# Performance work log

Measured on AMD Instinct MI355X. Metric: run time of the kernel, lower is better.

The kernel has to match this reference:

```python
import jax, jax.numpy as jnp
import numpy as np

MC = 16384
IND_T = 96
N_MAT = 4
N_STRIKES = 21


def _init_linear(key, fan_in, fan_out, prefix=()):
    k1, k2 = jax.random.split(key)
    lim = 1.0 / np.sqrt(fan_in)
    W = jax.random.uniform(k1, prefix + (fan_in, fan_out), minval=-lim, maxval=lim, dtype=jnp.float32)
    b = jax.random.uniform(k2, prefix + (fan_out,), minval=-lim, maxval=lim, dtype=jnp.float32)
    return W, b


def setup_inputs() -> dict:
    key = jax.random.key(0)
    ks = jax.random.split(key, 14)
    z = jax.random.normal(ks[0], (MC, IND_T), dtype=jnp.float32)
    zz = jax.random.normal(ks[1], (MC, IND_T), dtype=jnp.float32)
    timegrid = jnp.arange(IND_T + 1, dtype=jnp.float32) / 365.0  # daily grid
    maturities = jnp.array([24, 48, 72, 96], dtype=jnp.int32)    # in days
    strikes = jnp.linspace(0.8, 1.2, N_STRIKES, dtype=jnp.float32)
    sv_W1, sv_b1 = _init_linear(ks[2], 3, 100)
    sv_W2, sv_b2 = _init_linear(ks[3], 100, 100)
    sv_W3, sv_b3 = _init_linear(ks[4], 100, 1)
    vh_W1, vh_b1 = _init_linear(ks[5], 2, 20, (N_MAT,))
    vh_W2, vh_b2 = _init_linear(ks[6], 20, N_STRIKES, (N_MAT,))
    vd_W1, vd_b1 = _init_linear(ks[7], 1, 20)
    vd_W2, vd_b2 = _init_linear(ks[8], 20, 1)
    vv_W1, vv_b1 = _init_linear(ks[9], 1, 20)
    vv_W2, vv_b2 = _init_linear(ks[10], 20, 1)
    v0 = jax.random.uniform(ks[11], (1,), dtype=jnp.float32) * 0.1
    rho = jnp.ones((1,), dtype=jnp.float32) * -2.0
    return dict(S0=jnp.float32(1.0), rate=jnp.float32(0.05), z=z, zz=zz,
                timegrid=timegrid, strikes=strikes, v0=v0, rho=rho,
                sv_W1=sv_W1, sv_b1=sv_b1, sv_W2=sv_W2, sv_b2=sv_b2, sv_W3=sv_W3, sv_b3=sv_b3,
                vh_W1=vh_W1, vh_b1=vh_b1, vh_W2=vh_W2, vh_b2=vh_b2,
                vd_W1=vd_W1, vd_b1=vd_b1, vd_W2=vd_W2, vd_b2=vd_b2,
                vv_W1=vv_W1, vv_b1=vv_b1, vv_W2=vv_W2, vv_b2=vv_b2,
                maturities=maturities)


def reference(S0, rate, z, zz, timegrid, strikes, v0, rho,
              sv_W1, sv_b1, sv_W2, sv_b2, sv_W3, sv_b3,
              vh_W1, vh_b1, vh_W2, vh_b2,
              vd_W1, vd_b1, vd_W2, vd_b2,
              vv_W1, vv_b1, vv_W2, vv_b2,
              maturities):
    sg = jax.lax.stop_gradient
    mc = z.shape[0]
    n_mat = vh_W1.shape[0]
    n_strikes = strikes.shape[0]

    def s_vol(x):  # [MC,3] -> [MC,1], softplus output
        h1 = jax.nn.relu(x @ sv_W1 + sv_b1)
        h2 = jax.nn.relu(h1 @ sv_W2 + sv_b2)
        return jax.nn.softplus(h2 @ sv_W3 + sv_b3)

    def v_drift(v):  # [MC,1] -> [MC,1]
        return jax.nn.relu(v @ vd_W1 + vd_b1) @ vd_W2 + vd_b2

    def v_vol(v):  # [MC,1] -> [MC,1], softplus output
        return jax.nn.softplus(jax.nn.relu(v @ vv_W1 + vv_b1) @ vv_W2 + vv_b2)

    def vanilla_hedge_all(x):  # [MC,2] -> [MC, n_strikes, n_mat] (one net per maturity)
        h1 = jax.nn.relu(jnp.einsum('mi,kio->kmo', x, vh_W1) + vh_b1[:, None, :])
        out = jax.nn.softplus(jnp.einsum('kmo,koj->kmj', h1, vh_W2) + vh_b2[:, None, :])
        return jnp.transpose(out, (1, 2, 0))

    rho_t = jnp.tanh(rho)[0]
    days = jnp.round(timegrid * 365.0).astype(jnp.int32)       # [IND_T+1]
    le = days[1:, None] <= maturities[None, :]                  # [IND_T, n_mat]
    idx_net = jnp.argmax(le, axis=1)                            # first live maturity per step
    is_mat = jnp.any(days[1:, None] == maturities[None, :], axis=1)
    mat_idx = jnp.arange(n_mat)

    Slog0 = jnp.log(jnp.full((mc, 1), S0, dtype=jnp.float32))
    V0 = jnp.full((mc, 1), 1.0, dtype=jnp.float32) * jax.nn.sigmoid(v0)[0] * 0.5
    cv0 = jnp.zeros((mc, n_strikes, n_mat), dtype=jnp.float32)
    pv0 = jnp.zeros((n_mat, n_strikes), dtype=jnp.float32)

    xs = (z.T[:, :, None], zz.T[:, :, None], timegrid[:-1], timegrid[1:], idx_net, is_mat)

    def step(carry, x):
        Slog_old, V_old, cv, pv_h, pv_var = carry
        z_i, zz_i, t0, t1, idx, im = x
        h = t1 - t0
        sqh = jnp.sqrt(h)
        dW = sqh * z_i                                          # [MC,1]
        dB = rho_t * dW + jnp.sqrt(1.0 - rho_t ** 2) * sqh * zz_i
        ones_t = jnp.full((mc, 1), 1.0, dtype=jnp.float32) * t0
        pd = s_vol(jnp.concatenate([ones_t, Slog_old, V_old], axis=1))  # price diffusion
        cv_fwd = vanilla_hedge_all(jnp.concatenate([ones_t, sg(Slog_old)], axis=1))
        V_new = V_old + v_drift(V_old) * h + v_vol(V_old) * dB
        drift = rate - 0.5 * pd ** 2
        diff = pd * dW
        drift_c = 1.0 + jnp.abs(sg(drift)) * sqh                # tamed Euler
        diff_c = 1.0 + jnp.abs(sg(pd)) * sqh
        Slog_new = Slog_old + drift * h / drift_c + diff / diff_c
        S_new = jnp.exp(Slog_new)
        S_old = jnp.exp(Slog_old)
        dS = jnp.exp(-rate * t1) * S_new - jnp.exp(-rate * t0) * S_old  # [MC,1]
        mask = (mat_idx >= idx).astype(cv.dtype)                # live maturities only
        cv = cv + mask[None, None, :] * cv_fwd * sg(dS)[:, :, None]
        # hedged vanilla (call) prices collected at maturity steps
        payoff = jnp.exp(-rate * t1) * jnp.maximum(S_new - strikes[None, :], 0.0)
        price = payoff - cv[:, :, idx]                          # [MC, n_strikes]
        pv = jnp.mean(price, axis=0)
        pvar = jnp.var(price, axis=0, ddof=1)
        sel = (mat_idx == idx)[:, None] & im
        pv_h = jnp.where(sel, pv[None, :], pv_h)
        pv_var = jnp.where(sel, pvar[None, :], pv_var)
        return (Slog_new, V_new, cv, pv_h, pv_var), None

    (_, _, _, pv_h, pv_var), _ = jax.lax.scan(step, (Slog0, V0, cv0, pv0, pv0), xs)
    return jnp.stack([pv_h, pv_var])  # [2, n_mat, n_strikes]
```

## Files before the change

### kernel.cpp

```cpp
#include <hip/hip_runtime.h>
#include <hip/hip_bf16.h>
#include <math.h>


#define MC      16384
#define NSTEP   96
#define BLOCK   512
#define NGROUP  512
#define NPAIR   84

typedef short bf16x8 __attribute__((ext_vector_type(8)));
typedef float f32x4  __attribute__((ext_vector_type(4)));

union U8 { uint4 u; bf16x8 v; };
union BF2U { __hip_bfloat162 b; unsigned u; };

__device__ __forceinline__ unsigned bf16rne(float x) {
    unsigned u = __float_as_uint(x);
    return (u + 0x7FFFu + ((u >> 16) & 1u)) >> 16;
}
__device__ __forceinline__ unsigned pk2(float lo, float hi) {
    BF2U t; t.b = __float22bfloat162_rn(make_float2(lo, hi));
    return t.u;
}
__device__ __forceinline__ float sp(float x) {
    return fmaxf(x, 0.f) + __logf(1.f + __expf(-fabsf(x)));
}

__global__ __launch_bounds__(BLOCK, 4)
void lsv_sim(const float* __restrict__ S0p,   const float* __restrict__ ratep,
             const float* __restrict__ z,     const float* __restrict__ zzg,
             const float* __restrict__ strikesg,
             const float* __restrict__ v0p,   const float* __restrict__ rhop,
             const float* __restrict__ svW1,  const float* __restrict__ svb1,
             const float* __restrict__ svW2,  const float* __restrict__ svb2,
             const float* __restrict__ svW3,  const float* __restrict__ svb3,
             const float* __restrict__ vhW1,  const float* __restrict__ vhb1,
             const float* __restrict__ vhW2,  const float* __restrict__ vhb2,
             const float* __restrict__ vdW1,  const float* __restrict__ vdb1,
             const float* __restrict__ vdW2,  const float* __restrict__ vdb2,
             const float* __restrict__ vvW1,  const float* __restrict__ vvb1,
             const float* __restrict__ vvW2,  const float* __restrict__ vvb2,
             const int*   __restrict__ mats,
             float* __restrict__ psum, float* __restrict__ psq)
{
    __shared__ __align__(16) unsigned short H1c[16 * 32 * 8];
    __shared__ __align__(16) float W1f[16 * 32];
    __shared__ __align__(16) float WH1f[16 * 32];
    __shared__ __align__(16) float B2T[128], W3T[128];
    __shared__ __align__(16) float RED[32 * 4];
    __shared__ __align__(16) float VDl[2][32], VVl[2][32];
    __shared__ __align__(16) float PSs[2][32], PSq[2][32];
    __shared__ __align__(16) float VW[128];
    __shared__ __align__(16) float4 STEP[NSTEP];
    __shared__ float D1T[NSTEP];
    __shared__ int   ITAB[NSTEP];

    const int tid  = threadIdx.x;
    const int lane = tid & 63;
    const int w    = __builtin_amdgcn_readfirstlane(tid >> 6);
    const int quad = lane >> 4;
    const int col  = lane & 15;
    const int lp   = lane & 31;
    const int gpath = blockIdx.x * 32 + lp;

    const int pt = w & 1;
    const int jg = w >> 1;
    const int hm = w >> 1;

    for (int e = tid; e < 128; e += BLOCK) {
        float v = 0.f;
        if      (e < 20)             v = vdW1[e];
        else if (e < 40)             v = vdb1[e - 20];
        else if (e < 60)             v = vdW2[e - 40];
        else if (e >= 64 && e < 84)  v = vvW1[e - 64];
        else if (e >= 84 && e < 104) v = vvb1[e - 84];
        else if (e >= 104 && e < 124)v = vvW2[e - 104];
        else if (e == 124)           v = vdb2[0];
        else if (e == 125)           v = vvb2[0];
        VW[e] = v;
        B2T[e] = (e < 100) ? svb2[e] : 0.f;
        W3T[e] = (e < 100) ? svW3[e] : 0.f;
    }
    for (int e = tid; e < 512; e += BLOCK) {
        const int kc2 = e >> 5, r5 = e & 31, grp = r5 >> 3, kk = kc2 * 8 + (r5 & 7);
        float v = 0.f;
        if (kk < 100) v = (grp == 0) ? svW1[kk] : (grp == 1) ? svW1[100 + kk]
                        : (grp == 2) ? svW1[200 + kk] : svb1[kk];
        W1f[e] = v;
    }
    for (int e = tid; e < 512; e += BLOCK) {
        const int hq = e >> 5, r5 = e & 31, grp = r5 >> 3;
        const int hmm = hq >> 2, qq = hq & 3;
        const int j = qq * 8 + (r5 & 7);
        float v = 0.f;
        if (j < 20 && grp < 3)
            v = (grp == 0) ? vhW1[hmm * 40 + j] : (grp == 1) ? vhW1[hmm * 40 + 20 + j]
                                                : vhb1[hmm * 20 + j];
        WH1f[e] = v;
    }

    const float rate  = ratep[0];
    const float S0    = S0p[0];
    const float rho_t = tanhf(rhop[0]);
    const float srho  = sqrtf(1.f - rho_t * rho_t);
    const float b3    = svb3[0];

    if (tid < NSTEP) {
        const int i = tid;
        const float t0 = (float)i       * (1.f / 365.f);
        const float t1 = (float)(i + 1) * (1.f / 365.f);
        const float h  = t1 - t0;
        STEP[i] = make_float4(t0, h, sqrtf(h), __expf(-rate * t0));
        D1T[i]  = __expf(-rate * t1);
        const int day = i + 1;
        const int m0 = mats[0], m1 = mats[1], m2 = mats[2], m3 = mats[3];
        const int idx = (day > m0) + (day > m1) + (day > m2);
        const int mi  = (idx == 0) ? m0 : (idx == 1) ? m1 : (idx == 2) ? m2 : m3;
        ITAB[i] = idx | ((day == mi) ? 256 : 0);
    }

    bf16x8 Af[4][2];
#pragma unroll
    for (int c = 0; c < 4; c++)
#pragma unroll
        for (int t = 0; t < 2; t++) {
            U8 tt;
#pragma unroll
            for (int e2 = 0; e2 < 4; e2++) {
                const int k0 = 32 * c + 8 * quad + 2 * e2;
                const int j  = (2 * jg + t) * 16 + col;
                const float v0 = (k0     < 100 && j < 100) ? svW2[k0 * 100 + j]       : 0.f;
                const float v1 = (k0 + 1 < 100 && j < 100) ? svW2[(k0 + 1) * 100 + j] : 0.f;
                (&tt.u.x)[e2] = bf16rne(v0) | (bf16rne(v1) << 16);
            }
            Af[c][t] = tt.v;
        }
    bf16x8 Ah[2];
#pragma unroll
    for (int st = 0; st < 2; st++) {
        U8 tt;
#pragma unroll
        for (int e2 = 0; e2 < 4; e2++) {
            const int j0 = 8 * quad + 2 * e2, j1 = j0 + 1;
            const int s  = st * 16 + col;
            const float v0 = (j0 < 20 && s < 21) ? vhW2[hm * 420 + j0 * 21 + s] : 0.f;
            const float v1 = (j1 < 20 && s < 21) ? vhW2[hm * 420 + j1 * 21 + s] : 0.f;
            (&tt.u.x)[e2] = bf16rne(v0) | (bf16rne(v1) << 16);
        }
        Ah[st] = tt.v;
    }
    f32x4 c0h, c1h;
    float K0a[4], K1a[4];
#pragma unroll
    for (int r = 0; r < 4; r++) {
        const int s0 = quad * 4 + r, s1 = 16 + quad * 4 + r;
        c0h[r] = vhb2[hm * 21 + s0];
        K0a[r] = strikesg[s0];
        c1h[r] = (s1 < 21) ? vhb2[hm * 21 + s1] : 0.f;
        K1a[r] = (s1 < 21) ? strikesg[s1] : 1e30f;
    }

    float Slog = __logf(S0);
    float S    = __expf(Slog);
    float V    = (1.f / (1.f + __expf(-v0p[0]))) * 0.5f;
    f32x4 cv0 = {0.f, 0.f, 0.f, 0.f};
    f32x4 cv1 = {0.f, 0.f, 0.f, 0.f};
    float Slog_prev = 0.f, dS_prev = 0.f;

    const float* zrow  = z   + (size_t)gpath * NSTEP;
    const float* zzrow = zzg + (size_t)gpath * NSTEP;

    const int path = pt * 16 + col;
    const int kc   = jg * 4 + quad;

    __syncthreads();

    const int j0e = (2 * jg) * 16 + quad * 4;
    const float4 b2a = *reinterpret_cast<const float4*>(B2T + j0e);
    const float4 w3a = *reinterpret_cast<const float4*>(W3T + j0e);
    const float4 b2b = *reinterpret_cast<const float4*>(B2T + j0e + 16);
    const float4 w3b = *reinterpret_cast<const float4*>(W3T + j0e + 16);

    auto hedge_step = [&](int ip) {
        const int iv   = ITAB[ip];
        const int idxp = iv & 0xff;
        if (hm >= idxp) {
            const float t0p = STEP[ip].x;
            const float slp = __shfl(Slog_prev, path);
            U8 b;
#pragma unroll
            for (int hh = 0; hh < 2; hh++) {
                const float* Wp = WH1f + (hm * 4 + quad) * 32 + hh * 4;
                const float4 wt4 = *reinterpret_cast<const float4*>(Wp);
                const float4 ws4 = *reinterpret_cast<const float4*>(Wp + 8);
                const float4 bb4 = *reinterpret_cast<const float4*>(Wp + 16);
                const float x0 = fmaxf(bb4.x + t0p * wt4.x + slp * ws4.x, 0.f);
                const float x1 = fmaxf(bb4.y + t0p * wt4.y + slp * ws4.y, 0.f);
                const float x2 = fmaxf(bb4.z + t0p * wt4.z + slp * ws4.z, 0.f);
                const float x3 = fmaxf(bb4.w + t0p * wt4.w + slp * ws4.w, 0.f);
                (&b.u.x)[2 * hh]     = pk2(x0, x1);
                (&b.u.x)[2 * hh + 1] = pk2(x2, x3);
            }
            const f32x4 D0 = __builtin_amdgcn_mfma_f32_16x16x32_bf16(Ah[0], b.v, c0h, 0, 0, 0);
            const f32x4 D1 = __builtin_amdgcn_mfma_f32_16x16x32_bf16(Ah[1], b.v, c1h, 0, 0, 0);
            const float dsP = __shfl(dS_prev, path);
#pragma unroll
            for (int r = 0; r < 4; r++) {
                cv0[r] += sp(D0[r]) * dsP;
                cv1[r] += sp(D1[r]) * dsP;
            }
            if ((iv & 256) && hm == idxp) {
                const float Sp   = __shfl(S, path);
                const float d1p  = D1T[ip];
                float p0[4], q0[4], p1[4], q1[4];
#pragma unroll
                for (int r = 0; r < 4; r++) {
                    p0[r] = d1p * fmaxf(Sp - K0a[r], 0.f) - cv0[r];
                    p1[r] = d1p * fmaxf(Sp - K1a[r], 0.f) - cv1[r];
                    q0[r] = p0[r] * p0[r];
                    q1[r] = p1[r] * p1[r];
                }
#pragma unroll
                for (int o = 1; o <= 8; o <<= 1) {
#pragma unroll
                    for (int r = 0; r < 4; r++) {
                        p0[r] += __shfl_xor(p0[r], o);
                        q0[r] += __shfl_xor(q0[r], o);
                        p1[r] += __shfl_xor(p1[r], o);
                        q1[r] += __shfl_xor(q1[r], o);
                    }
                }
                if (col == 0) {
#pragma unroll
                    for (int r = 0; r < 4; r++) {
                        const int s0 = quad * 4 + r, s1 = 16 + quad * 4 + r;
                        PSs[pt][s0] = p0[r];  PSq[pt][s0] = q0[r];
                        if (s1 < 21) { PSs[pt][s1] = p1[r];  PSq[pt][s1] = q1[r]; }
                    }
                }
            }
        }
    };

    auto ps_reduce = [&](int ip) {
        if (w == 0) {
            const int iv = ITAB[ip];
            if (iv & 256) {
                const int s = lane & 31;
                if (s < 21) {
                    const float* src = (lane >= 32) ? &PSq[0][0] : &PSs[0][0];
                    const float acc = src[s] + src[32 + s];
                    float* dst = (lane >= 32) ? psq : psum;
                    dst[((iv & 0xff) * 21 + s) * NGROUP + blockIdx.x] = acc;
                }
            }
        }
    };

    for (int i = 0; i < NSTEP; i++) {
        const float zi  = zrow[i];
        const float zzi = zzrow[i];
        const float4 u  = STEP[i];

        {
            const float slp = __shfl(Slog, path);
            const float vp  = __shfl(V, path);
            const float t0  = u.x;
            const float* Wp = W1f + kc * 32;
            uint4 o;
#pragma unroll
            for (int hh = 0; hh < 2; hh++) {
                const float4 a4 = *reinterpret_cast<const float4*>(Wp + hh * 4);
                const float4 b4 = *reinterpret_cast<const float4*>(Wp + 8 + hh * 4);
                const float4 c4 = *reinterpret_cast<const float4*>(Wp + 16 + hh * 4);
                const float4 d4 = *reinterpret_cast<const float4*>(Wp + 24 + hh * 4);
                const float x0 = fmaxf(d4.x + t0 * a4.x + slp * b4.x + vp * c4.x, 0.f);
                const float x1 = fmaxf(d4.y + t0 * a4.y + slp * b4.y + vp * c4.y, 0.f);
                const float x2 = fmaxf(d4.z + t0 * a4.z + slp * b4.z + vp * c4.z, 0.f);
                const float x3 = fmaxf(d4.w + t0 * a4.w + slp * b4.w + vp * c4.w, 0.f);
                (&o.x)[2 * hh]     = pk2(x0, x1);
                (&o.x)[2 * hh + 1] = pk2(x2, x3);
            }
            *reinterpret_cast<uint4*>(H1c + (kc * 32 + path) * 8) = o;
        }
        if (i > 0) hedge_step(i - 1);
        if (w == 0) {
            float a2 = 0.f;
#pragma unroll
            for (int q5 = 0; q5 < 5; q5++) {
                const float4 w1 = *reinterpret_cast<const float4*>(VW + 4 * q5);
                const float4 b1 = *reinterpret_cast<const float4*>(VW + 20 + 4 * q5);
                const float4 w2 = *reinterpret_cast<const float4*>(VW + 40 + 4 * q5);
                a2 += fmaxf(V * w1.x + b1.x, 0.f) * w2.x;
                a2 += fmaxf(V * w1.y + b1.y, 0.f) * w2.y;
                a2 += fmaxf(V * w1.z + b1.z, 0.f) * w2.z;
                a2 += fmaxf(V * w1.w + b1.w, 0.f) * w2.w;
            }
            if (lane < 32) VDl[i & 1][lane] = a2;
        }
        if (w == 1) {
            float a2 = 0.f;
#pragma unroll
            for (int q5 = 0; q5 < 5; q5++) {
                const float4 w1 = *reinterpret_cast<const float4*>(VW + 64 + 4 * q5);
                const float4 b1 = *reinterpret_cast<const float4*>(VW + 84 + 4 * q5);
                const float4 w2 = *reinterpret_cast<const float4*>(VW + 104 + 4 * q5);
                a2 += fmaxf(V * w1.x + b1.x, 0.f) * w2.x;
                a2 += fmaxf(V * w1.y + b1.y, 0.f) * w2.y;
                a2 += fmaxf(V * w1.z + b1.z, 0.f) * w2.z;
                a2 += fmaxf(V * w1.w + b1.w, 0.f) * w2.w;
            }
            if (lane < 32) VVl[i & 1][lane] = a2;
        }
        __syncthreads();

        {
            f32x4 d0 = {0.f, 0.f, 0.f, 0.f};
            f32x4 d1 = {0.f, 0.f, 0.f, 0.f};
#pragma unroll
            for (int c = 0; c < 4; c++) {
                const bf16x8 b = *reinterpret_cast<const bf16x8*>(
                    H1c + ((quad + 4 * c) * 32 + path) * 8);
                d0 = __builtin_amdgcn_mfma_f32_16x16x32_bf16(Af[c][0], b, d0, 0, 0, 0);
                d1 = __builtin_amdgcn_mfma_f32_16x16x32_bf16(Af[c][1], b, d1, 0, 0, 0);
            }
            float acc = fmaxf(d0[0] + b2a.x, 0.f) * w3a.x
                      + fmaxf(d0[1] + b2a.y, 0.f) * w3a.y
                      + fmaxf(d0[2] + b2a.z, 0.f) * w3a.z
                      + fmaxf(d0[3] + b2a.w, 0.f) * w3a.w
                      + fmaxf(d1[0] + b2b.x, 0.f) * w3b.x
                      + fmaxf(d1[1] + b2b.y, 0.f) * w3b.y
                      + fmaxf(d1[2] + b2b.z, 0.f) * w3b.z
                      + fmaxf(d1[3] + b2b.w, 0.f) * w3b.w;
            acc += __shfl_xor(acc, 16);
            acc += __shfl_xor(acc, 32);
            if (quad == 0)
                RED[path * 4 + jg] = acc;
        }
        if (i > 0) ps_reduce(i - 1);
        __syncthreads();

        {
            const float4 rr = *reinterpret_cast<const float4*>(RED + lp * 4);
            const float pout = (rr.x + rr.y) + (rr.z + rr.w);
            const float pd = sp(pout + b3);
            const float vdv = VDl[i & 1][lp] + VW[124];
            const float vvv = sp(VVl[i & 1][lp] + VW[125]);
            const float sqh = u.z;
            const float dW = sqh * zi;
            const float dB = rho_t * dW + srho * sqh * zzi;
            const float Vn = V + vdv * u.y + vvv * dB;
            const float drift   = rate - 0.5f * pd * pd;
            const float diff    = pd * dW;
            const float drift_c = 1.f + fabsf(drift) * sqh;
            const float diff_c  = 1.f + fabsf(pd) * sqh;
            const float Sln = Slog + __fdividef(drift * u.y, drift_c) + __fdividef(diff, diff_c);
            const float Sn  = __expf(Sln);
            const float dS  = D1T[i] * Sn - u.w * S;
            Slog_prev = Slog; dS_prev = dS;
            Slog = Sln; S = Sn; V = Vn;
        }
    }

    hedge_step(NSTEP - 1);
    __syncthreads();
    ps_reduce(NSTEP - 1);
}

__global__ void lsv_finalize(const float* __restrict__ psum,
                             const float* __restrict__ psq,
                             float* __restrict__ out)
{
    const int t    = blockIdx.x;
    const int lane = threadIdx.x;
    float s = 0.f, q = 0.f;
    for (int b = lane; b < NGROUP; b += 64) {
        s += psum[t * NGROUP + b];
        q += psq [t * NGROUP + b];
    }
#pragma unroll
    for (int o = 1; o <= 32; o <<= 1) {
        s += __shfl_xor(s, o);
        q += __shfl_xor(q, o);
    }
    if (lane == 0) {
        const float mean = s * (1.0f / (float)MC);
        const float var  = (q - (float)MC * mean * mean) * (1.0f / (float)(MC - 1));
        out[t]         = mean;
        out[NPAIR + t] = var;
    }
}

extern "C" void kernel_launch(void* const* d_in, const int* in_sizes, int n_in,
                              void* d_out, int out_size, void* d_ws, size_t ws_size,
                              hipStream_t stream)
{
    const float* S0    = (const float*)d_in[0];
    const float* rate  = (const float*)d_in[1];
    const float* z     = (const float*)d_in[2];
    const float* zz    = (const float*)d_in[3];
    const float* strikes = (const float*)d_in[5];
    const float* v0    = (const float*)d_in[6];
    const float* rho   = (const float*)d_in[7];
    const float* svW1  = (const float*)d_in[8];
    const float* svb1  = (const float*)d_in[9];
    const float* svW2  = (const float*)d_in[10];
    const float* svb2  = (const float*)d_in[11];
    const float* svW3  = (const float*)d_in[12];
    const float* svb3  = (const float*)d_in[13];
    const float* vhW1  = (const float*)d_in[14];
    const float* vhb1  = (const float*)d_in[15];
    const float* vhW2  = (const float*)d_in[16];
    const float* vhb2  = (const float*)d_in[17];
    const float* vdW1  = (const float*)d_in[18];
    const float* vdb1  = (const float*)d_in[19];
    const float* vdW2  = (const float*)d_in[20];
    const float* vdb2  = (const float*)d_in[21];
    const float* vvW1  = (const float*)d_in[22];
    const float* vvb1  = (const float*)d_in[23];
    const float* vvW2  = (const float*)d_in[24];
    const float* vvb2  = (const float*)d_in[25];
    const int*   mats  = (const int*)d_in[26];

    float* psum = (float*)d_ws;
    float* psq  = psum + NPAIR * NGROUP;

    hipLaunchKernelGGL(lsv_sim, dim3(NGROUP), dim3(BLOCK), 0, stream,
                       S0, rate, z, zz, strikes, v0, rho,
                       svW1, svb1, svW2, svb2, svW3, svb3,
                       vhW1, vhb1, vhW2, vhb2,
                       vdW1, vdb1, vdW2, vdb2,
                       vvW1, vvb1, vvW2, vvb2,
                       mats, psum, psq);

    hipLaunchKernelGGL(lsv_finalize, dim3(NPAIR), dim3(64), 0, stream,
                       psum, psq, (float*)d_out);
}
```

Measured before the change: 435.7 us.

## Stage noise in LDS, precompute time-dependent layer terms, centralize state update in one wave

Preloads each block's z and zz rows into shared memory so the step loop no longer issues global loads. The time-dependent bias terms of the first layers are precomputed into double-buffered shared arrays by otherwise idle waves. The per-path state update now runs only in wave 1, which broadcasts the state through shared memory instead of shuffles. The two small vol nets are merged into a single wave. This adds an extra __syncthreads per step and more LDS use, which may reduce occupancy and add barrier latency.

```diff
diff --git a/kernel.cpp b/kernel.cpp
--- a/kernel.cpp
+++ b/kernel.cpp
@@ -49,12 +49,16 @@
     __shared__ __align__(16) float WH1f[16 * 32];
     __shared__ __align__(16) float B2T[128], W3T[128];
     __shared__ __align__(16) float RED[32 * 4];
-    __shared__ __align__(16) float VDl[2][32], VVl[2][32];
-    __shared__ __align__(16) float PSs[2][32], PSq[2][32];
+    __shared__ float VDl[32], VVl[32];
+    __shared__ float PSs[2][32], PSq[2][32];
     __shared__ __align__(16) float VW[128];
     __shared__ __align__(16) float4 STEP[NSTEP];
     __shared__ float D1T[NSTEP];
     __shared__ int   ITAB[NSTEP];
+    __shared__ float ZT[32][97], ZZT[32][97];
+    __shared__ float SLOG[32], VST[32], SST[32], SLOGP[32], DSP[32];
+    __shared__ __align__(16) float CW1[2][128];
+    __shared__ __align__(16) float CH[2][128];
 
     const int tid  = threadIdx.x;
     const int lane = tid & 63;
@@ -62,12 +66,19 @@
     const int quad = lane >> 4;
     const int col  = lane & 15;
     const int lp   = lane & 31;
-    const int gpath = blockIdx.x * 32 + lp;
 
     const int pt = w & 1;
     const int jg = w >> 1;
     const int hm = w >> 1;
 
+    {
+        const size_t gbase = (size_t)blockIdx.x * 32 * NSTEP;
+        for (int e = tid; e < 32 * NSTEP; e += BLOCK) {
+            const int p = e / NSTEP, ii = e - p * NSTEP;
+            ZT[p][ii]  = z  [gbase + e];
+            ZZT[p][ii] = zzg[gbase + e];
+        }
+    }
     for (int e = tid; e < 128; e += BLOCK) {
         float v = 0.f;
         if      (e < 20)             v = vdW1[e];
@@ -166,13 +177,28 @@
     float V    = (1.f / (1.f + __expf(-v0p[0]))) * 0.5f;
     f32x4 cv0 = {0.f, 0.f, 0.f, 0.f};
     f32x4 cv1 = {0.f, 0.f, 0.f, 0.f};
-    float Slog_prev = 0.f, dS_prev = 0.f;
-
-    const float* zrow  = z   + (size_t)gpath * NSTEP;
-    const float* zzrow = zzg + (size_t)gpath * NSTEP;
 
     const int path = pt * 16 + col;
     const int kc   = jg * 4 + quad;
+
+    __syncthreads();
+
+    if (tid < 128) {
+        const float t00 = STEP[0].x;
+        const int kk = tid;
+        CW1[0][kk] = fmaf(t00, W1f[(kk >> 3) * 32 + (kk & 7)],
+                               W1f[(kk >> 3) * 32 + 24 + (kk & 7)]);
+    } else if (tid < 256) {
+        const float t00 = STEP[0].x;
+        const int e = tid - 128;
+        CH[0][e] = fmaf(t00, WH1f[(e >> 3) * 32 + (e & 7)],
+                             WH1f[(e >> 3) * 32 + 16 + (e & 7)]);
+    }
+    if (tid < 32) {
+        SLOG[tid] = Slog;
+        SST[tid]  = S;
+        VST[tid]  = V;
+    }
 
     __syncthreads();
 
@@ -186,33 +212,32 @@
         const int iv   = ITAB[ip];
         const int idxp = iv & 0xff;
         if (hm >= idxp) {
-            const float t0p = STEP[ip].x;
-            const float slp = __shfl(Slog_prev, path);
+            const int hb = ip & 1;
+            const float slp = SLOGP[path];
             U8 b;
 #pragma unroll
             for (int hh = 0; hh < 2; hh++) {
-                const float* Wp = WH1f + (hm * 4 + quad) * 32 + hh * 4;
-                const float4 wt4 = *reinterpret_cast<const float4*>(Wp);
-                const float4 ws4 = *reinterpret_cast<const float4*>(Wp + 8);
-                const float4 bb4 = *reinterpret_cast<const float4*>(Wp + 16);
-                const float x0 = fmaxf(bb4.x + t0p * wt4.x + slp * ws4.x, 0.f);
-                const float x1 = fmaxf(bb4.y + t0p * wt4.y + slp * ws4.y, 0.f);
-                const float x2 = fmaxf(bb4.z + t0p * wt4.z + slp * ws4.z, 0.f);
-                const float x3 = fmaxf(bb4.w + t0p * wt4.w + slp * ws4.w, 0.f);
+                const float* Wp = WH1f + (hm * 4 + quad) * 32 + 8 + hh * 4;
+                const float4 ws4 = *reinterpret_cast<const float4*>(Wp);
+                const float4 ch4 = *reinterpret_cast<const float4*>(&CH[hb][(hm * 4 + quad) * 8 + hh * 4]);
+                const float x0 = fmaxf(ch4.x + slp * ws4.x, 0.f);
+                const float x1 = fmaxf(ch4.y + slp * ws4.y, 0.f);
+                const float x2 = fmaxf(ch4.z + slp * ws4.z, 0.f);
+                const float x3 = fmaxf(ch4.w + slp * ws4.w, 0.f);
                 (&b.u.x)[2 * hh]     = pk2(x0, x1);
                 (&b.u.x)[2 * hh + 1] = pk2(x2, x3);
             }
             const f32x4 D0 = __builtin_amdgcn_mfma_f32_16x16x32_bf16(Ah[0], b.v, c0h, 0, 0, 0);
             const f32x4 D1 = __builtin_amdgcn_mfma_f32_16x16x32_bf16(Ah[1], b.v, c1h, 0, 0, 0);
-            const float dsP = __shfl(dS_prev, path);
+            const float dsP = DSP[path];
 #pragma unroll
             for (int r = 0; r < 4; r++) {
                 cv0[r] += sp(D0[r]) * dsP;
                 cv1[r] += sp(D1[r]) * dsP;
             }
             if ((iv & 256) && hm == idxp) {
-                const float Sp   = __shfl(S, path);
-                const float d1p  = D1T[ip];
+                const float Sp  = SST[path];
+                const float d1p = D1T[ip];
                 float p0[4], q0[4], p1[4], q1[4];
 #pragma unroll
                 for (int r = 0; r < 4; r++) {
@@ -259,26 +284,22 @@
     };
 
     for (int i = 0; i < NSTEP; i++) {
-        const float zi  = zrow[i];
-        const float zzi = zzrow[i];
-        const float4 u  = STEP[i];
+        const int buf = i & 1;
 
         {
-            const float slp = __shfl(Slog, path);
-            const float vp  = __shfl(V, path);
-            const float t0  = u.x;
+            const float slp = SLOG[path];
+            const float vp  = VST[path];
             const float* Wp = W1f + kc * 32;
             uint4 o;
 #pragma unroll
             for (int hh = 0; hh < 2; hh++) {
-                const float4 a4 = *reinterpret_cast<const float4*>(Wp + hh * 4);
                 const float4 b4 = *reinterpret_cast<const float4*>(Wp + 8 + hh * 4);
                 const float4 c4 = *reinterpret_cast<const float4*>(Wp + 16 + hh * 4);
-                const float4 d4 = *reinterpret_cast<const float4*>(Wp + 24 + hh * 4);
-                const float x0 = fmaxf(d4.x + t0 * a4.x + slp * b4.x + vp * c4.x, 0.f);
-                const float x1 = fmaxf(d4.y + t0 * a4.y + slp * b4.y + vp * c4.y, 0.f);
-                const float x2 = fmaxf(d4.z + t0 * a4.z + slp * b4.z + vp * c4.z, 0.f);
-                const float x3 = fmaxf(d4.w + t0 * a4.w + slp * b4.w + vp * c4.w, 0.f);
+                const float4 cw = *reinterpret_cast<const float4*>(&CW1[buf][kc * 8 + hh * 4]);
+                const float x0 = fmaxf(cw.x + slp * b4.x + vp * c4.x, 0.f);
+                const float x1 = fmaxf(cw.y + slp * b4.y + vp * c4.y, 0.f);
+                const float x2 = fmaxf(cw.z + slp * b4.z + vp * c4.z, 0.f);
+                const float x3 = fmaxf(cw.w + slp * b4.w + vp * c4.w, 0.f);
                 (&o.x)[2 * hh]     = pk2(x0, x1);
                 (&o.x)[2 * hh + 1] = pk2(x2, x3);
             }
@@ -286,32 +307,20 @@
         }
         if (i > 0) hedge_step(i - 1);
         if (w == 0) {
+            const float Vp = VST[lp];
+            const float* bw = VW + ((lane >= 32) ? 64 : 0);
             float a2 = 0.f;
 #pragma unroll
             for (int q5 = 0; q5 < 5; q5++) {
-                const float4 w1 = *reinterpret_cast<const float4*>(VW + 4 * q5);
-                const float4 b1 = *reinterpret_cast<const float4*>(VW + 20 + 4 * q5);
-                const float4 w2 = *reinterpret_cast<const float4*>(VW + 40 + 4 * q5);
-                a2 += fmaxf(V * w1.x + b1.x, 0.f) * w2.x;
-                a2 += fmaxf(V * w1.y + b1.y, 0.f) * w2.y;
-                a2 += fmaxf(V * w1.z + b1.z, 0.f) * w2.z;
-                a2 += fmaxf(V * w1.w + b1.w, 0.f) * w2.w;
-            }
-            if (lane < 32) VDl[i & 1][lane] = a2;
-        }
-        if (w == 1) {
-            float a2 = 0.f;
-#pragma unroll
-            for (int q5 = 0; q5 < 5; q5++) {
-                const float4 w1 = *reinterpret_cast<const float4*>(VW + 64 + 4 * q5);
-                const float4 b1 = *reinterpret_cast<const float4*>(VW + 84 + 4 * q5);
-                const float4 w2 = *reinterpret_cast<const float4*>(VW + 104 + 4 * q5);
-                a2 += fmaxf(V * w1.x + b1.x, 0.f) * w2.x;
-                a2 += fmaxf(V * w1.y + b1.y, 0.f) * w2.y;
-                a2 += fmaxf(V * w1.z + b1.z, 0.f) * w2.z;
-                a2 += fmaxf(V * w1.w + b1.w, 0.f) * w2.w;
-            }
-            if (lane < 32) VVl[i & 1][lane] = a2;
+                const float4 w1 = *reinterpret_cast<const float4*>(bw + 4 * q5);
+                const float4 b1 = *reinterpret_cast<const float4*>(bw + 20 + 4 * q5);
+                const float4 w2 = *reinterpret_cast<const float4*>(bw + 40 + 4 * q5);
+                a2 += fmaxf(Vp * w1.x + b1.x, 0.f) * w2.x;
+                a2 += fmaxf(Vp * w1.y + b1.y, 0.f) * w2.y;
+                a2 += fmaxf(Vp * w1.z + b1.z, 0.f) * w2.z;
+                a2 += fmaxf(Vp * w1.w + b1.w, 0.f) * w2.w;
+            }
+            if (lane < 32) VDl[lp] = a2; else VVl[lp] = a2;
         }
         __syncthreads();
 
@@ -341,13 +350,16 @@
         if (i > 0) ps_reduce(i - 1);
         __syncthreads();
 
-        {
+        if (w == 1) {
             const float4 rr = *reinterpret_cast<const float4*>(RED + lp * 4);
             const float pout = (rr.x + rr.y) + (rr.z + rr.w);
             const float pd = sp(pout + b3);
-            const float vdv = VDl[i & 1][lp] + VW[124];
-            const float vvv = sp(VVl[i & 1][lp] + VW[125]);
+            const float vdv = VDl[lp] + VW[124];
+            const float vvv = sp(VVl[lp] + VW[125]);
+            const float4 u  = STEP[i];
             const float sqh = u.z;
+            const float zi  = ZT[lp][i];
+            const float zzi = ZZT[lp][i];
             const float dW = sqh * zi;
             const float dB = rho_t * dW + srho * sqh * zzi;
             const float Vn = V + vdv * u.y + vvv * dB;
@@ -358,9 +370,23 @@
             const float Sln = Slog + __fdividef(drift * u.y, drift_c) + __fdividef(diff, diff_c);
             const float Sn  = __expf(Sln);
             const float dS  = D1T[i] * Sn - u.w * S;
-            Slog_prev = Slog; dS_prev = dS;
+            if (lane < 32) {
+                SLOGP[lp] = Slog;  DSP[lp] = dS;
+                SLOG[lp]  = Sln;   SST[lp] = Sn;  VST[lp] = Vn;
+            }
             Slog = Sln; S = Sn; V = Vn;
-        }
+        } else if ((w == 2 || w == 3) && i + 1 < NSTEP) {
+            const float t0n = STEP[i + 1].x;
+            const int kk = (w - 2) * 64 + lane;
+            CW1[buf ^ 1][kk] = fmaf(t0n, W1f[(kk >> 3) * 32 + (kk & 7)],
+                                         W1f[(kk >> 3) * 32 + 24 + (kk & 7)]);
+        } else if ((w == 4 || w == 5) && i + 1 < NSTEP) {
+            const float t0n = STEP[i + 1].x;
+            const int e = (w - 4) * 64 + lane;
+            CH[buf ^ 1][e] = fmaf(t0n, WH1f[(e >> 3) * 32 + (e & 7)],
+                                       WH1f[(e >> 3) * 32 + 16 + (e & 7)]);
+        }
+        __syncthreads();
     }
 
     hedge_step(NSTEP - 1);
```

Result: faster. 392.3 us (-9.9%).
